# Kernel tuning notes

Hardware: AMD Instinct MI355X
Metric: run time of the kernel (lower is better)

Reference implementation:

```python
import jax, jax.numpy as jnp
import numpy as np
from jax import lax

B, T, D_LAT, D, H, J = 2048, 60, 100, 512, 256, 6
LRELU_SLOPE = 0.2
BN_EPS = 1e-5

# --- fixed kinematic-chain constants (stand-in for URDF: 6-DoF right arm) ---
AXES = np.array([[0,0,1],[1,0,0],[0,1,0],[1,0,0],[0,1,0],[1,0,0]], np.float32)
OFFS = np.array([[0,0,0.10],[0,0,0],[0,0,0],[0,-0.25,0],[0,0,0],[0,-0.25,0]], np.float32)
LOWER = np.array([-3.1416,-1.5708,-3.1416,-2.6,-1.5708,-1.2], np.float32)
UPPER = np.array([ 3.1416, 1.5708, 3.1416, 0.1, 1.5708, 1.2], np.float32)
FING1 = np.array([0.0,-0.08, 0.02], np.float32)
FING4 = np.array([0.0,-0.08,-0.02], np.float32)

def _skew(a):
    return np.array([[0,-a[2],a[1]],[a[2],0,-a[0]],[-a[1],a[0],0]], np.float32)

def fk_batch(joints):
    """joints: [B,T,6] normalized in [0,1]-ish -> poses [B,T,3,3]."""
    th = joints * (UPPER - LOWER) + LOWER                      # denormalize
    bt = th.shape[:2]
    R = jnp.broadcast_to(jnp.eye(3, dtype=th.dtype), bt + (3, 3))
    p = jnp.zeros(bt + (3,), th.dtype)
    pos = []
    for j in range(J):
        K = jnp.asarray(_skew(AXES[j]))
        a = th[..., j][..., None, None]
        Rj = jnp.eye(3, dtype=th.dtype) + jnp.sin(a) * K + (1.0 - jnp.cos(a)) * (K @ K)
        p = p + jnp.einsum('btij,j->bti', R, jnp.asarray(OFFS[j]))  # Trans then Rot
        R = jnp.einsum('btij,btjk->btik', R, Rj)
        pos.append(p)
    shoulder2, forearm, wrist = pos[1], pos[3], pos[5]
    f1 = wrist + jnp.einsum('btij,j->bti', R, jnp.asarray(FING1))
    f4 = wrist + jnp.einsum('btij,j->bti', R, jnp.asarray(FING4))
    body_L = (jnp.linalg.norm(shoulder2 - forearm, axis=-1)
              + jnp.linalg.norm(wrist - forearm, axis=-1)) * 0.5   # [B,T]
    rel = jnp.stack([wrist - shoulder2, f1 - shoulder2, f4 - shoulder2], axis=2)
    return rel / body_L[..., None, None]

def gru_dir(x, Wih, Whh, bih, bhh, reverse):
    xg = jnp.einsum('btd,gd->btg', x, Wih) + bih               # [B,T,3H]
    xg = jnp.swapaxes(xg, 0, 1)                                 # [T,B,3H]
    def step(h, g):
        gh = h @ Whh.T + bhh
        r = jax.nn.sigmoid(g[:, :H] + gh[:, :H])
        zz = jax.nn.sigmoid(g[:, H:2*H] + gh[:, H:2*H])
        n = jnp.tanh(g[:, 2*H:] + r * gh[:, 2*H:])
        hn = (1.0 - zz) * n + zz * h
        return hn, hn
    h0 = jnp.zeros((x.shape[0], H), x.dtype)
    _, ys = lax.scan(step, h0, xg, reverse=reverse)
    return jnp.swapaxes(ys, 0, 1)                               # [B,T,H]

def setup_inputs() -> dict:
    key = jax.random.key(0)
    ks = jax.random.split(key, 12)
    s = 0.05
    inp = {
        'z': jax.random.normal(ks[0], (B, D_LAT), jnp.float32),
        'W_fc': jax.random.normal(ks[1], (D, D_LAT), jnp.float32) * s,
        'b_fc': jnp.zeros((D,), jnp.float32),
        'bn_g': jnp.ones((D,), jnp.float32),
        'bn_b': jnp.zeros((D,), jnp.float32),
        'Wih_f': jax.random.normal(ks[2], (3*H, D), jnp.float32) * s,
        'Whh_f': jax.random.normal(ks[3], (3*H, H), jnp.float32) * s,
        'bih_f': jnp.zeros((3*H,), jnp.float32),
        'bhh_f': jnp.zeros((3*H,), jnp.float32),
        'Wih_b': jax.random.normal(ks[4], (3*H, D), jnp.float32) * s,
        'Whh_b': jax.random.normal(ks[5], (3*H, H), jnp.float32) * s,
        'bih_b': jnp.zeros((3*H,), jnp.float32),
        'bhh_b': jnp.zeros((3*H,), jnp.float32),
        'attn_W1': jax.random.normal(ks[6], (H, 2*H), jnp.float32) * s,
        'attn_b1': jnp.zeros((H,), jnp.float32),
        'attn_W2': jax.random.normal(ks[7], (H,), jnp.float32) * s,
        'joint_W': jax.random.normal(ks[8], (J, 2*H), jnp.float32) * s,
        'joint_b': jnp.zeros((J,), jnp.float32),
    }
    return inp

def reference(z, W_fc, b_fc, bn_g, bn_b, Wih_f, Whh_f, bih_f, bhh_f,
              Wih_b, Whh_b, bih_b, bhh_b, attn_W1, attn_b1, attn_W2,
              joint_W, joint_b):
    # fc: Linear + BatchNorm1d (training-mode batch stats) + LeakyReLU(0.2)
    h0 = z @ W_fc.T + b_fc                                      # [B,512]
    mu = jnp.mean(h0, axis=0)
    var = jnp.mean((h0 - mu) ** 2, axis=0)
    hb = (h0 - mu) * jax.lax.rsqrt(var + BN_EPS) * bn_g + bn_b
    h = jnp.where(hb >= 0, hb, LRELU_SLOPE * hb)
    x = jnp.broadcast_to(h[:, None, :], (h.shape[0], T, D))     # repeat over seq
    # bidirectional GRU
    gf = gru_dir(x, Wih_f, Whh_f, bih_f, bhh_f, False)
    gb = gru_dir(x, Wih_b, Whh_b, bih_b, bhh_b, True)
    gru_out = jnp.concatenate([gf, gb], axis=-1)                # [B,T,512]
    # attention over time
    a = jnp.tanh(jnp.einsum('btd,hd->bth', gru_out, attn_W1) + attn_b1)
    w = jax.nn.softmax(jnp.einsum('bth,h->bt', a, attn_W2), axis=1)[..., None]
    c = jnp.sum(w * gru_out, axis=1, keepdims=True)             # [B,1,512]
    joints = jnp.einsum('btd,jd->btj', gru_out + c, joint_W) + joint_b
    return fk_batch(joints)                                     # [B,T,3,3]
```

## Files before the change

### kernel.cpp

```cpp
#include <hip/hip_runtime.h>
#include <hip/hip_fp16.h>

#define NB 2048
#define NT 60
#define NDL 100
#define ND 512
#define NH 256
#define NG 768

#define L2E  1.44269504f
#define L2E2 2.88539008f

typedef const float* __restrict__ fpp;
typedef _Float16 half8 __attribute__((ext_vector_type(8)));
typedef float floatx4 __attribute__((ext_vector_type(4)));

__device__ __forceinline__ float fast_rcp(float x) {
  return __builtin_amdgcn_rcpf(x);
}
__device__ __forceinline__ float fast_exp2(float x) {
#if __has_builtin(__builtin_amdgcn_exp2f)
  return __builtin_amdgcn_exp2f(x);
#else
  return exp2f(x);
#endif
}
__device__ __forceinline__ float fsin(float x) {
#if __has_builtin(__builtin_amdgcn_sinf)
  return __builtin_amdgcn_sinf(x * 0.15915494309189535f);
#else
  return __sinf(x);
#endif
}
__device__ __forceinline__ float fcos(float x) {
#if __has_builtin(__builtin_amdgcn_cosf)
  return __builtin_amdgcn_cosf(x * 0.15915494309189535f);
#else
  return __cosf(x);
#endif
}

__global__ __launch_bounds__(256) void gemm_fc(
    fpp A, fpp Bm, fpp bias, float* __restrict__ C,
    int M, int N, int K, int lda, int ldb, int ldc)
{
  __shared__ float As[16][68];
  __shared__ float Bs[16][68];
  const int bm = blockIdx.x * 64, bn = blockIdx.y * 64;
  const int tid = threadIdx.x;
  const int tx = tid & 15, ty = tid >> 4;
  float acc[4][4] = {};
  for (int k0 = 0; k0 < K; k0 += 16) {
#pragma unroll
    for (int i = 0; i < 4; i++) {
      int e = tid + i * 256;
      int m = e >> 4, k = e & 15;
      As[k][m] = (k0 + k < K) ? A[(size_t)(bm + m) * lda + k0 + k] : 0.f;
      Bs[k][m] = (k0 + k < K) ? Bm[(size_t)(bn + m) * ldb + k0 + k] : 0.f;
    }
    __syncthreads();
#pragma unroll
    for (int kk = 0; kk < 16; kk++) {
      float4 av = *(const float4*)&As[kk][ty * 4];
      float4 bv = *(const float4*)&Bs[kk][tx * 4];
      float a_[4] = {av.x, av.y, av.z, av.w};
      float b_[4] = {bv.x, bv.y, bv.z, bv.w};
#pragma unroll
      for (int i = 0; i < 4; i++)
#pragma unroll
        for (int j = 0; j < 4; j++)
          acc[i][j] = fmaf(a_[i], b_[j], acc[i][j]);
    }
    __syncthreads();
  }
#pragma unroll
  for (int i = 0; i < 4; i++) {
    int m = bm + ty * 4 + i;
#pragma unroll
    for (int j = 0; j < 4; j++) {
      int n = bn + tx * 4 + j;
      C[(size_t)m * ldc + n] = acc[i][j] + bias[n];
    }
  }
}

__global__ __launch_bounds__(256) void bn_partial(
    const float* __restrict__ h0, float* __restrict__ s1g,
    float* __restrict__ s2g)
{
  const int r0 = blockIdx.x * 32;
  const int tid = threadIdx.x;
  float a1 = 0.f, a2 = 0.f, b1 = 0.f, b2 = 0.f;
  for (int r = 0; r < 32; r++) {
    float v = h0[(size_t)(r0 + r) * ND + tid];
    float w = h0[(size_t)(r0 + r) * ND + tid + 256];
    a1 += v; a2 += v * v;
    b1 += w; b2 += w * w;
  }
  atomicAdd(&s1g[tid], a1);
  atomicAdd(&s2g[tid], a2);
  atomicAdd(&s1g[tid + 256], b1);
  atomicAdd(&s2g[tid + 256], b2);
}

__global__ void bn_lrelu_h16(const float* __restrict__ h0,
                             fpp g, fpp b,
                             const float* __restrict__ s1g,
                             const float* __restrict__ s2g,
                             __half* __restrict__ h16g)
{
  int idx = blockIdx.x * 256 + threadIdx.x;
  int d = idx & (ND - 1);
  float mu = s1g[d] * (1.f / NB);
  float var = s2g[d] * (1.f / NB) - mu * mu;
  float sc = g[d] * rsqrtf(var + 1e-5f);
  float sh = b[d] - mu * sc;
  float v = h0[idx] * sc + sh;
  h16g[idx] = __float2half(v >= 0.f ? v : 0.2f * v);
}

__global__ void convert_w(fpp whf, fpp whb, fpp w1, fpp wif, fpp wib, fpp jw,
                          __half* __restrict__ o_whf, __half* __restrict__ o_whb,
                          __half* __restrict__ o_w1, __half* __restrict__ o_wif,
                          __half* __restrict__ o_wib, __half* __restrict__ o_jw)
{
  int idx = blockIdx.x * 256 + threadIdx.x;
  if (idx < 196608) {
    float s = ((idx >> 16) == 2) ? L2E2 : L2E;
    o_whf[idx] = __float2half(whf[idx] * s);
  } else if (idx < 393216) {
    int e = idx - 196608;
    float s = ((e >> 16) == 2) ? L2E2 : L2E;
    o_whb[e] = __float2half(whb[e] * s);
  } else if (idx < 524288) {
    int e = idx - 393216;
    o_w1[e] = __float2half(w1[e] * L2E2);
  } else if (idx < 917504) {
    int e = idx - 524288;
    float s = ((e >> 17) == 2) ? L2E2 : L2E;
    o_wif[e] = __float2half(wif[e] * s);
  } else if (idx < 1310720) {
    int e = idx - 917504;
    float s = ((e >> 17) == 2) ? L2E2 : L2E;
    o_wib[e] = __float2half(wib[e] * s);
  } else if (idx < 1318912) {
    int e = idx - 1310720;
    o_jw[e] = (e < 6 * ND) ? __float2half(jw[e]) : __float2half(0.f);
  }
}

__global__ __launch_bounds__(256) void gemm16_dual(
    const __half* __restrict__ A,
    const __half* __restrict__ B0, const __half* __restrict__ B1,
    fpp bias0, fpp bias1, float* __restrict__ C0, float* __restrict__ C1,
    int N, int K)
{
  const __half* __restrict__ Bm = blockIdx.z ? B1 : B0;
  fpp bias = blockIdx.z ? bias1 : bias0;
  float* __restrict__ C = blockIdx.z ? C1 : C0;

  __shared__ __half As[64 * 40];
  __shared__ __half Bs[64 * 40];
  const int bm = blockIdx.x * 64, bn = blockIdx.y * 64;
  const int tid = threadIdx.x;
  const int wave = tid >> 6, lane = tid & 63;
  const int lm = lane & 15, quad = lane >> 4;
  floatx4 acc[4];
#pragma unroll
  for (int nt = 0; nt < 4; nt++) acc[nt] = (floatx4){0.f, 0.f, 0.f, 0.f};

  const int row = tid >> 2, kc = tid & 3;
  for (int k0 = 0; k0 < K; k0 += 32) {
    __syncthreads();
    *(float4*)&As[row * 40 + kc * 8] =
      *(const float4*)&A[(size_t)(bm + row) * K + k0 + kc * 8];
    *(float4*)&Bs[row * 40 + kc * 8] =
      *(const float4*)&Bm[(size_t)(bn + row) * K + k0 + kc * 8];
    __syncthreads();
    half8 af = *(const half8*)&As[(wave * 16 + lm) * 40 + quad * 8];
#pragma unroll
    for (int nt = 0; nt < 4; nt++) {
      half8 bf = *(const half8*)&Bs[(nt * 16 + lm) * 40 + quad * 8];
      acc[nt] = __builtin_amdgcn_mfma_f32_16x16x32_f16(af, bf, acc[nt], 0, 0, 0);
    }
  }
#pragma unroll
  for (int nt = 0; nt < 4; nt++) {
    int n = bn + nt * 16 + lm;
    float bv = bias[n] * ((n < 2 * NH) ? L2E : L2E2);
#pragma unroll
    for (int r = 0; r < 4; r++) {
      int m = bm + wave * 16 + quad * 4 + r;
      C[(size_t)m * N + n] = acc[nt][r] + bv;
    }
  }
}

__global__ __launch_bounds__(512, 2) void gru_persistent(
    const float* __restrict__ xg_f, const float* __restrict__ xg_b,
    const __half* __restrict__ whh16_f, const __half* __restrict__ whh16_b,
    fpp bhh_f, fpp bhh_b, __half* __restrict__ seq)
{
  const int dir  = blockIdx.x & 1;
  const int tile = blockIdx.x >> 1;
  const int bm   = tile * 16;
  const float* __restrict__ xg = dir ? xg_b : xg_f;
  const __half* __restrict__ Whh = dir ? whh16_b : whh16_f;
  fpp bhh = dir ? bhh_b : bhh_f;
  const int dcol = dir * NH;
  const int tid = threadIdx.x;
  const int wave = tid >> 6, lane = tid & 63;
  const int lm = lane & 15, quad = lane >> 4;
  const int n0 = wave * 32;

  __shared__ __half h16s[2][16 * 264];
  __shared__ __half wts[96 * 512];

  floatx4 breg[3][2][6];
  {
    const __half* bp[3][2];
#pragma unroll
    for (int g = 0; g < 3; g++)
#pragma unroll
      for (int c = 0; c < 2; c++)
        bp[g][c] = Whh + (size_t)(g * NH + n0 + c * 16 + lm) * NH + quad * 8;

#pragma unroll
    for (int g = 0; g < 3; g++)
#pragma unroll
      for (int c = 0; c < 2; c++)
#pragma unroll
        for (int kb = 0; kb < 6; kb++)
          breg[g][c][kb] = *(const floatx4*)(bp[g][c] + kb * 32);
#pragma unroll
    for (int g = 0; g < 3; g++)
#pragma unroll
      for (int c = 0; c < 2; c++)
#pragma unroll
        for (int kb = 0; kb < 6; kb++)
          asm volatile("" : "+v"(breg[g][c][kb]));

#pragma unroll
    for (int g = 0; g < 3; g++)
#pragma unroll
      for (int c = 0; c < 2; c++)
#pragma unroll
        for (int k2 = 0; k2 < 2; k2++)
          *(float4*)&wts[(wave * 12 + g * 4 + c * 2 + k2) * 512 + lane * 8] =
            *(const float4*)(bp[g][c] + 192 + k2 * 32);
  }

  float xr_[2][4], xz_[2][4], xn_[2][4];
  float bn_[2];
#pragma unroll
  for (int c = 0; c < 2; c++) {
    int n = n0 + c * 16 + lm;
    float br = bhh[n] * L2E, bz = bhh[NH + n] * L2E;
    bn_[c] = bhh[2 * NH + n] * L2E2;
#pragma unroll
    for (int r = 0; r < 4; r++) {
      int m = bm + quad * 4 + r;
      const float* xp = xg + (size_t)m * NG + n;
      xr_[c][r] = xp[0] + br;
      xz_[c][r] = xp[NH] + bz;
      xn_[c][r] = xp[2 * NH];
    }
  }

  float hp[2][4];
#pragma unroll
  for (int c = 0; c < 2; c++)
#pragma unroll
    for (int r = 0; r < 4; r++) hp[c][r] = 0.f;

  const int arow = lm * 264 + quad * 8;
  const int cm = tid >> 5, cpart = tid & 31;
  const int wb = wave * 6144 + lane * 8;

  __half* seqp = seq + ((size_t)(bm + cm) * NT + (dir ? NT - 1 : 0)) * ND
                 + dcol + cpart * 8;
  const ptrdiff_t seqd = dir ? -(ptrdiff_t)ND : (ptrdiff_t)ND;

  for (int step = 0; step < NT; step++) {
    const int cur = step & 1, prv = cur ^ 1;
    __half* __restrict__ hCur = h16s[cur];
    const __half* __restrict__ hPrv = h16s[prv];
    floatx4 acc[3][2];

    if (step > 0) {
      {
        float4 v = *(const float4*)&hPrv[cm * 264 + cpart * 8];
        *(float4*)seqp = v;
        seqp += seqd;
      }
      half8 b6[3][2], b7[3][2];
#pragma unroll
      for (int g = 0; g < 3; g++)
#pragma unroll
        for (int c = 0; c < 2; c++) {
          const __half* wp = &wts[wb + (g * 4 + c * 2) * 512];
          b6[g][c] = *(const half8*)wp;
          b7[g][c] = *(const half8*)(wp + 512);
        }
      {
        half8 a = *(const half8*)&hPrv[arow];
#pragma unroll
        for (int g = 0; g < 3; g++)
#pragma unroll
          for (int c = 0; c < 2; c++)
            acc[g][c] = __builtin_amdgcn_mfma_f32_16x16x32_f16(
                a, __builtin_bit_cast(half8, breg[g][c][0]),
                (floatx4){0.f, 0.f, 0.f, 0.f}, 0, 0, 0);
      }
#pragma unroll
      for (int kb = 1; kb < 6; kb++) {
        half8 a = *(const half8*)&hPrv[arow + kb * 32];
#pragma unroll
        for (int g = 0; g < 3; g++)
#pragma unroll
          for (int c = 0; c < 2; c++)
            acc[g][c] = __builtin_amdgcn_mfma_f32_16x16x32_f16(
                a, __builtin_bit_cast(half8, breg[g][c][kb]), acc[g][c], 0, 0, 0);
      }
      {
        half8 a = *(const half8*)&hPrv[arow + 192];
#pragma unroll
        for (int g = 0; g < 3; g++)
#pragma unroll
          for (int c = 0; c < 2; c++)
            acc[g][c] = __builtin_amdgcn_mfma_f32_16x16x32_f16(a, b6[g][c], acc[g][c], 0, 0, 0);
      }
      {
        half8 a = *(const half8*)&hPrv[arow + 224];
#pragma unroll
        for (int g = 0; g < 3; g++)
#pragma unroll
          for (int c = 0; c < 2; c++)
            acc[g][c] = __builtin_amdgcn_mfma_f32_16x16x32_f16(a, b7[g][c], acc[g][c], 0, 0, 0);
      }
    } else {
#pragma unroll
      for (int g = 0; g < 3; g++)
#pragma unroll
        for (int c = 0; c < 2; c++) acc[g][c] = (floatx4){0.f, 0.f, 0.f, 0.f};
    }

#pragma unroll
    for (int c = 0; c < 2; c++) {
      int n = n0 + c * 16 + lm;
#pragma unroll
      for (int r = 0; r < 4; r++) {
        int m = quad * 4 + r;
        float rg = fast_rcp(1.f + fast_exp2(-(xr_[c][r] + acc[0][c][r])));
        float zg = fast_rcp(1.f + fast_exp2(-(xz_[c][r] + acc[1][c][r])));
        float t  = fast_exp2(fmaf(rg, acc[2][c][r] + bn_[c], xn_[c][r]));
        float nn = fmaf(-2.f, fast_rcp(t + 1.f), 1.f);
        float hv = fmaf(zg, hp[c][r] - nn, nn);
        hp[c][r] = hv;
        hCur[m * 264 + n] = __float2half(hv);
      }
    }
    __syncthreads();
  }

  {
    const __half* hLast = h16s[(NT - 1) & 1];
    float4 v = *(const float4*)&hLast[cm * 264 + cpart * 8];
    *(float4*)seqp = v;
  }
}

__global__ __launch_bounds__(256) void attn_score_mfma(
    const __half* __restrict__ seq, const __half* __restrict__ w116,
    const __half* __restrict__ jw16, fpp b1, fpp W2,
    float* __restrict__ scores, float* __restrict__ gJ)
{
  const int bm = blockIdx.x * 128;
  const int tid = threadIdx.x;
  const int wave = tid >> 6, lane = tid & 63;
  const int lm = lane & 15, quad = lane >> 4;
  const int mh = wave & 1;
  const int nh = wave >> 1;

  __shared__ __half As[128 * 40];
  __shared__ __half Bs[256 * 40];
  __shared__ __half Js[16 * 40];
  __shared__ float partial[2][128];

  floatx4 acc[4][8];
  floatx4 accJ[4];
#pragma unroll
  for (int t = 0; t < 4; t++) {
#pragma unroll
    for (int u = 0; u < 8; u++) acc[t][u] = (floatx4){0.f, 0.f, 0.f, 0.f};
    accJ[t] = (floatx4){0.f, 0.f, 0.f, 0.f};
  }

  for (int k0 = 0; k0 < ND; k0 += 32) {
    __syncthreads();
#pragma unroll
    for (int i = 0; i < 2; i++) {
      int e = tid + i * 256;
      int row = e >> 2, kc = e & 3;
      *(float4*)&As[row * 40 + kc * 8] =
        *(const float4*)&seq[(size_t)(bm + row) * ND + k0 + kc * 8];
    }
#pragma unroll
    for (int i = 0; i < 4; i++) {
      int e = tid + i * 256;
      int row = e >> 2, kc = e & 3;
      *(float4*)&Bs[row * 40 + kc * 8] =
        *(const float4*)&w116[(size_t)row * ND + k0 + kc * 8];
    }
    if (tid < 64) {
      int row = tid >> 2, kc = tid & 3;
      *(float4*)&Js[row * 40 + kc * 8] =
        *(const float4*)&jw16[(size_t)row * ND + k0 + kc * 8];
    }
    __syncthreads();
    half8 a[4];
#pragma unroll
    for (int t = 0; t < 4; t++)
      a[t] = *(const half8*)&As[((mh * 4 + t) * 16 + lm) * 40 + quad * 8];
#pragma unroll
    for (int u = 0; u < 8; u++) {
      half8 bf = *(const half8*)&Bs[((nh * 8 + u) * 16 + lm) * 40 + quad * 8];
#pragma unroll
      for (int t = 0; t < 4; t++)
        acc[t][u] = __builtin_amdgcn_mfma_f32_16x16x32_f16(a[t], bf, acc[t][u], 0, 0, 0);
    }
    if (nh == 1) {
      half8 bj = *(const half8*)&Js[lm * 40 + quad * 8];
#pragma unroll
      for (int t = 0; t < 4; t++)
        accJ[t] = __builtin_amdgcn_mfma_f32_16x16x32_f16(a[t], bj, accJ[t], 0, 0, 0);
    }
  }

  float rs[4][4] = {};
#pragma unroll
  for (int u = 0; u < 8; u++) {
    int n = (nh * 8 + u) * 16 + lm;
    float b1v = b1[n] * L2E2, w2v = W2[n];
#pragma unroll
    for (int t = 0; t < 4; t++)
#pragma unroll
      for (int r = 0; r < 4; r++) {
        float tt = fast_exp2(acc[t][u][r] + b1v);
        float th = fmaf(-2.f, fast_rcp(tt + 1.f), 1.f);
        rs[t][r] = fmaf(th, w2v, rs[t][r]);
      }
  }
#pragma unroll
  for (int t = 0; t < 4; t++)
#pragma unroll
    for (int r = 0; r < 4; r++) {
      rs[t][r] += __shfl_xor(rs[t][r], 1);
      rs[t][r] += __shfl_xor(rs[t][r], 2);
      rs[t][r] += __shfl_xor(rs[t][r], 4);
      rs[t][r] += __shfl_xor(rs[t][r], 8);
    }
  if (lm == 0) {
#pragma unroll
    for (int t = 0; t < 4; t++)
#pragma unroll
      for (int r = 0; r < 4; r++)
        partial[nh][mh * 64 + t * 16 + quad * 4 + r] = rs[t][r];
  }
  if (nh == 1) {
#pragma unroll
    for (int t = 0; t < 4; t++)
#pragma unroll
      for (int r = 0; r < 4; r++) {
        int row = bm + mh * 64 + t * 16 + quad * 4 + r;
        gJ[(size_t)row * 16 + lm] = accJ[t][r];
      }
  }
  __syncthreads();
  if (tid < 128) scores[bm + tid] = partial[0][tid] + partial[1][tid];
}

__constant__ float c_lower[6] = {-3.1416f, -1.5708f, -3.1416f, -2.6f, -1.5708f, -1.2f};
__constant__ float c_upper[6] = { 3.1416f,  1.5708f,  3.1416f,  0.1f,  1.5708f,  1.2f};

__global__ __launch_bounds__(64) void attn_post(
    const float* __restrict__ scores_in, const float* __restrict__ gJ,
    fpp jb, float* __restrict__ out)
{
  const int b = blockIdx.x;
  const int t = threadIdx.x;

  float v = (t < NT) ? scores_in[(size_t)b * NT + t] : -1e30f;
  float m = v;
#pragma unroll
  for (int off = 32; off >= 1; off >>= 1) m = fmaxf(m, __shfl_xor(m, off));
  float e = (t < NT) ? __expf(v - m) : 0.f;
  float sum = e;
#pragma unroll
  for (int off = 32; off >= 1; off >>= 1) sum += __shfl_xor(sum, off);
  float w = e * fast_rcp(sum);

  __shared__ float gj[NT * 16];
  __shared__ float wl[64];
  __shared__ float cj[16];
  wl[t] = w;
  const float* gsrc = gJ + (size_t)b * NT * 16;
#pragma unroll
  for (int i = 0; i < 15; i++) gj[t + i * 64] = gsrc[t + i * 64];
  __syncthreads();

  if (t < 16) {
    float s = 0.f;
    for (int tt = 0; tt < NT; tt++) s += wl[tt] * gj[tt * 16 + t];
    cj[t] = s;
  }
  __syncthreads();

  if (t >= NT) return;

  float th[6];
#pragma unroll
  for (int j = 0; j < 6; j++) {
    float jnt = gj[t * 16 + j] + cj[j] + jb[j];
    th[j] = jnt * (c_upper[j] - c_lower[j]) + c_lower[j];
  }

  float c0x = 1.f, c0y = 0.f, c0z = 0.f;
  float c1x = 0.f, c1y = 1.f, c1z = 0.f;
  float c2x = 0.f, c2y = 0.f, c2z = 1.f;
  float px = 0.f, py = 0.f, pz = 0.1f;
  float s, cc, tx_, ty_, tz_, ux_, uy_, uz_;

  s = fsin(th[0]); cc = fcos(th[0]);
  tx_ = cc * c0x + s * c1x; ty_ = cc * c0y + s * c1y; tz_ = cc * c0z + s * c1z;
  ux_ = -s * c0x + cc * c1x; uy_ = -s * c0y + cc * c1y; uz_ = -s * c0z + cc * c1z;
  c0x = tx_; c0y = ty_; c0z = tz_; c1x = ux_; c1y = uy_; c1z = uz_;

  float shx = px, shy = py, shz = pz;
  s = fsin(th[1]); cc = fcos(th[1]);
  tx_ = cc * c1x + s * c2x; ty_ = cc * c1y + s * c2y; tz_ = cc * c1z + s * c2z;
  ux_ = -s * c1x + cc * c2x; uy_ = -s * c1y + cc * c2y; uz_ = -s * c1z + cc * c2z;
  c1x = tx_; c1y = ty_; c1z = tz_; c2x = ux_; c2y = uy_; c2z = uz_;

  s = fsin(th[2]); cc = fcos(th[2]);
  tx_ = cc * c0x - s * c2x; ty_ = cc * c0y - s * c2y; tz_ = cc * c0z - s * c2z;
  ux_ = s * c0x + cc * c2x; uy_ = s * c0y + cc * c2y; uz_ = s * c0z + cc * c2z;
  c0x = tx_; c0y = ty_; c0z = tz_; c2x = ux_; c2y = uy_; c2z = uz_;

  px -= 0.25f * c1x; py -= 0.25f * c1y; pz -= 0.25f * c1z;
  float fox = px, foy = py, foz = pz;
  s = fsin(th[3]); cc = fcos(th[3]);
  tx_ = cc * c1x + s * c2x; ty_ = cc * c1y + s * c2y; tz_ = cc * c1z + s * c2z;
  ux_ = -s * c1x + cc * c2x; uy_ = -s * c1y + cc * c2y; uz_ = -s * c1z + cc * c2z;
  c1x = tx_; c1y = ty_; c1z = tz_; c2x = ux_; c2y = uy_; c2z = uz_;

  s = fsin(th[4]); cc = fcos(th[4]);
  tx_ = cc * c0x - s * c2x; ty_ = cc * c0y - s * c2y; tz_ = cc * c0z - s * c2z;
  ux_ = s * c0x + cc * c2x; uy_ = s * c0y + cc * c2y; uz_ = s * c0z + cc * c2z;
  c0x = tx_; c0y = ty_; c0z = tz_; c2x = ux_; c2y = uy_; c2z = uz_;

  px -= 0.25f * c1x; py -= 0.25f * c1y; pz -= 0.25f * c1z;
  float wx = px, wy = py, wz = pz;
  s = fsin(th[5]); cc = fcos(th[5]);
  tx_ = cc * c1x + s * c2x; ty_ = cc * c1y + s * c2y; tz_ = cc * c1z + s * c2z;
  ux_ = -s * c1x + cc * c2x; uy_ = -s * c1y + cc * c2y; uz_ = -s * c1z + cc * c2z;
  c1x = tx_; c1y = ty_; c1z = tz_; c2x = ux_; c2y = uy_; c2z = uz_;

  float f1x = wx - 0.08f * c1x + 0.02f * c2x;
  float f1y = wy - 0.08f * c1y + 0.02f * c2y;
  float f1z = wz - 0.08f * c1z + 0.02f * c2z;
  float f4x = wx - 0.08f * c1x - 0.02f * c2x;
  float f4y = wy - 0.08f * c1y - 0.02f * c2y;
  float f4z = wz - 0.08f * c1z - 0.02f * c2z;

  float dsx = shx - fox, dsy = shy - foy, dsz = shz - foz;
  float dwx = wx - fox, dwy = wy - foy, dwz = wz - foz;
  float bodyL = 0.5f * (sqrtf(dsx * dsx + dsy * dsy + dsz * dsz) +
                        sqrtf(dwx * dwx + dwy * dwy + dwz * dwz));
  float inv = fast_rcp(bodyL);

  float* o = out + ((size_t)b * NT + t) * 9;
  o[0] = (wx - shx) * inv; o[1] = (wy - shy) * inv; o[2] = (wz - shz) * inv;
  o[3] = (f1x - shx) * inv; o[4] = (f1y - shy) * inv; o[5] = (f1z - shz) * inv;
  o[6] = (f4x - shx) * inv; o[7] = (f4y - shy) * inv; o[8] = (f4z - shz) * inv;
}

extern "C" void kernel_launch(void* const* d_in, const int* in_sizes, int n_in,
                              void* d_out, int out_size, void* d_ws, size_t ws_size,
                              hipStream_t stream)
{
  fpp z     = (fpp)d_in[0];
  fpp W_fc  = (fpp)d_in[1];
  fpp b_fc  = (fpp)d_in[2];
  fpp bn_g  = (fpp)d_in[3];
  fpp bn_b  = (fpp)d_in[4];
  fpp Wih_f = (fpp)d_in[5];
  fpp Whh_f = (fpp)d_in[6];
  fpp bih_f = (fpp)d_in[7];
  fpp bhh_f = (fpp)d_in[8];
  fpp Wih_b = (fpp)d_in[9];
  fpp Whh_b = (fpp)d_in[10];
  fpp bih_b = (fpp)d_in[11];
  fpp bhh_b = (fpp)d_in[12];
  fpp aW1   = (fpp)d_in[13];
  fpp ab1   = (fpp)d_in[14];
  fpp aW2   = (fpp)d_in[15];
  fpp jW    = (fpp)d_in[16];
  fpp jb    = (fpp)d_in[17];

  float* ws     = (float*)d_ws;
  float* h0     = ws;
  float* xg_f   = h0 + 1048576;
  float* xg_b   = xg_f + 1572864;
  float* bns1   = xg_b + 1572864;
  float* bns2   = bns1 + 512;
  float* scores = bns2 + 512;
  float* cbuf   = scores + 122880;
  __half* gseq    = (__half*)(cbuf + 1048576);
  __half* whh16_f = gseq + 62914560;
  __half* whh16_b = whh16_f + 196608;
  __half* w116    = whh16_b + 196608;
  __half* wih16_f = w116 + 131072;
  __half* wih16_b = wih16_f + 393216;
  __half* h16g    = wih16_b + 393216;
  __half* jw16    = h16g + 1048576;
  float*  gJ      = (float*)(jw16 + 8192);

  convert_w<<<5152, 256, 0, stream>>>(Whh_f, Whh_b, aW1, Wih_f, Wih_b, jW,
                                      whh16_f, whh16_b, w116, wih16_f, wih16_b,
                                      jw16);
  hipMemsetAsync(bns1, 0, 1024 * sizeof(float), stream);
  gemm_fc<<<dim3(32, 8), 256, 0, stream>>>(z, W_fc, b_fc, h0,
                                           NB, ND, NDL, NDL, NDL, ND);
  bn_partial<<<64, 256, 0, stream>>>(h0, bns1, bns2);
  bn_lrelu_h16<<<4096, 256, 0, stream>>>(h0, bn_g, bn_b, bns1, bns2, h16g);
  gemm16_dual<<<dim3(32, 12, 2), 256, 0, stream>>>(
      h16g, wih16_f, wih16_b, bih_f, bih_b, xg_f, xg_b, NG, ND);
  gru_persistent<<<256, 512, 0, stream>>>(xg_f, xg_b, whh16_f, whh16_b,
                                          bhh_f, bhh_b, gseq);
  attn_score_mfma<<<960, 256, 0, stream>>>(gseq, w116, jw16, ab1, aW2,
                                           scores, gJ);
  attn_post<<<NB, 64, 0, stream>>>(scores, gJ, jb, (float*)d_out);
}
```

Baseline: 330.6 us.

## Interleave GRU matmul chains with gate math and prefetch attention tiles

The GRU recurrence now preloads the x-gate terms and hidden bias into the MFMA accumulators and runs the matmul for column chunk 0, then its gates, then chunk 1 and its gates. s_setprio is used so one wave's gate math can overlap another wave's MFMAs. The gate formula is rewritten algebraically to use fewer reciprocals. The attention-score kernel register-prefetches the next K tile from global memory while the current tile is being computed. The aim is to shorten the serial per-step critical path and hide global load latency, at the cost of more registers and changed fp rounding.

```diff
diff --git a/kernel.cpp b/kernel.cpp
--- a/kernel.cpp
+++ b/kernel.cpp
@@ -196,6 +196,47 @@
   }
 }
 
+#define GATES(C) do {                                                        \
+    _Pragma("unroll")                                                        \
+    for (int r = 0; r < 4; r++) {                                            \
+      float er = fast_exp2(-acc[0][C][r]);                                   \
+      float rg = fast_rcp(1.f + er);                                         \
+      float ez = fast_exp2(-acc[1][C][r]);                                   \
+      float tt = fast_exp2(fmaf(rg, acc[2][C][r], xn4[C][r]));               \
+      float dd = tt + 1.f;                                                   \
+      float num = fmaf(tt, ez + hp[C][r], hp[C][r] - ez);                    \
+      float den = fmaf(dd, ez, dd);                                          \
+      float hv = num * fast_rcp(den);                                        \
+      hp[C][r] = hv;                                                         \
+      hCur[(quad * 4 + r) * 264 + (n0 + C * 16 + lm)] = __float2half(hv);    \
+    }                                                                        \
+  } while (0)
+
+#define CHAIN(C) do {                                                        \
+    half8 t6[3], t7[3];                                                      \
+    _Pragma("unroll")                                                        \
+    for (int g = 0; g < 3; g++) {                                            \
+      const __half* wp = &wts[wb + (g * 4 + C * 2) * 512];                   \
+      t6[g] = *(const half8*)wp;                                             \
+      t7[g] = *(const half8*)(wp + 512);                                     \
+    }                                                                        \
+    _Pragma("unroll")                                                        \
+    for (int kb = 0; kb < 6; kb++)                                           \
+      _Pragma("unroll")                                                      \
+      for (int g = 0; g < 3; g++)                                            \
+        acc[g][C] = __builtin_amdgcn_mfma_f32_16x16x32_f16(                  \
+            a[kb], __builtin_bit_cast(half8, breg[g][C][kb]), acc[g][C],     \
+            0, 0, 0);                                                        \
+    _Pragma("unroll")                                                        \
+    for (int g = 0; g < 3; g++)                                              \
+      acc[g][C] = __builtin_amdgcn_mfma_f32_16x16x32_f16(                    \
+          a[6], t6[g], acc[g][C], 0, 0, 0);                                  \
+    _Pragma("unroll")                                                        \
+    for (int g = 0; g < 3; g++)                                              \
+      acc[g][C] = __builtin_amdgcn_mfma_f32_16x16x32_f16(                    \
+          a[7], t7[g], acc[g][C], 0, 0, 0);                                  \
+  } while (0)
+
 __global__ __launch_bounds__(512, 2) void gru_persistent(
     const float* __restrict__ xg_f, const float* __restrict__ xg_b,
     const __half* __restrict__ whh16_f, const __half* __restrict__ whh16_b,
@@ -250,7 +291,7 @@
             *(const float4*)(bp[g][c] + 192 + k2 * 32);
   }
 
-  float xr_[2][4], xz_[2][4], xn_[2][4];
+  floatx4 xr4[2], xz4[2], xn4[2];
   float bn_[2];
 #pragma unroll
   for (int c = 0; c < 2; c++) {
@@ -261,9 +302,9 @@
     for (int r = 0; r < 4; r++) {
       int m = bm + quad * 4 + r;
       const float* xp = xg + (size_t)m * NG + n;
-      xr_[c][r] = xp[0] + br;
-      xz_[c][r] = xp[NH] + bz;
-      xn_[c][r] = xp[2 * NH];
+      xr4[c][r] = xp[0] + br;
+      xz4[c][r] = xp[NH] + bz;
+      xn4[c][r] = xp[2 * NH];
     }
   }
 
@@ -286,6 +327,12 @@
     __half* __restrict__ hCur = h16s[cur];
     const __half* __restrict__ hPrv = h16s[prv];
     floatx4 acc[3][2];
+#pragma unroll
+    for (int c = 0; c < 2; c++) {
+      acc[0][c] = xr4[c];
+      acc[1][c] = xz4[c];
+      acc[2][c] = (floatx4){bn_[c], bn_[c], bn_[c], bn_[c]};
+    }
 
     if (step > 0) {
       {
@@ -293,72 +340,22 @@
         *(float4*)seqp = v;
         seqp += seqd;
       }
-      half8 b6[3][2], b7[3][2];
-#pragma unroll
-      for (int g = 0; g < 3; g++)
-#pragma unroll
-        for (int c = 0; c < 2; c++) {
-          const __half* wp = &wts[wb + (g * 4 + c * 2) * 512];
-          b6[g][c] = *(const half8*)wp;
-          b7[g][c] = *(const half8*)(wp + 512);
-        }
-      {
-        half8 a = *(const half8*)&hPrv[arow];
-#pragma unroll
-        for (int g = 0; g < 3; g++)
-#pragma unroll
-          for (int c = 0; c < 2; c++)
-            acc[g][c] = __builtin_amdgcn_mfma_f32_16x16x32_f16(
-                a, __builtin_bit_cast(half8, breg[g][c][0]),
-                (floatx4){0.f, 0.f, 0.f, 0.f}, 0, 0, 0);
-      }
-#pragma unroll
-      for (int kb = 1; kb < 6; kb++) {
-        half8 a = *(const half8*)&hPrv[arow + kb * 32];
-#pragma unroll
-        for (int g = 0; g < 3; g++)
-#pragma unroll
-          for (int c = 0; c < 2; c++)
-            acc[g][c] = __builtin_amdgcn_mfma_f32_16x16x32_f16(
-                a, __builtin_bit_cast(half8, breg[g][c][kb]), acc[g][c], 0, 0, 0);
-      }
-      {
-        half8 a = *(const half8*)&hPrv[arow + 192];
-#pragma unroll
-        for (int g = 0; g < 3; g++)
-#pragma unroll
-          for (int c = 0; c < 2; c++)
-            acc[g][c] = __builtin_amdgcn_mfma_f32_16x16x32_f16(a, b6[g][c], acc[g][c], 0, 0, 0);
-      }
-      {
-        half8 a = *(const half8*)&hPrv[arow + 224];
-#pragma unroll
-        for (int g = 0; g < 3; g++)
-#pragma unroll
-          for (int c = 0; c < 2; c++)
-            acc[g][c] = __builtin_amdgcn_mfma_f32_16x16x32_f16(a, b7[g][c], acc[g][c], 0, 0, 0);
-      }
+      half8 a[8];
+#pragma unroll
+      for (int kb = 0; kb < 8; kb++)
+        a[kb] = *(const half8*)&hPrv[arow + kb * 32];
+
+      __builtin_amdgcn_s_setprio(1);
+      CHAIN(0);
+      __builtin_amdgcn_s_setprio(0);
+      GATES(0);
+      __builtin_amdgcn_s_setprio(1);
+      CHAIN(1);
+      __builtin_amdgcn_s_setprio(0);
+      GATES(1);
     } else {
-#pragma unroll
-      for (int g = 0; g < 3; g++)
-#pragma unroll
-        for (int c = 0; c < 2; c++) acc[g][c] = (floatx4){0.f, 0.f, 0.f, 0.f};
-    }
-
-#pragma unroll
-    for (int c = 0; c < 2; c++) {
-      int n = n0 + c * 16 + lm;
-#pragma unroll
-      for (int r = 0; r < 4; r++) {
-        int m = quad * 4 + r;
-        float rg = fast_rcp(1.f + fast_exp2(-(xr_[c][r] + acc[0][c][r])));
-        float zg = fast_rcp(1.f + fast_exp2(-(xz_[c][r] + acc[1][c][r])));
-        float t  = fast_exp2(fmaf(rg, acc[2][c][r] + bn_[c], xn_[c][r]));
-        float nn = fmaf(-2.f, fast_rcp(t + 1.f), 1.f);
-        float hv = fmaf(zg, hp[c][r] - nn, nn);
-        hp[c][r] = hv;
-        hCur[m * 264 + n] = __float2half(hv);
-      }
+      GATES(0);
+      GATES(1);
     }
     __syncthreads();
   }
@@ -396,28 +393,32 @@
     accJ[t] = (floatx4){0.f, 0.f, 0.f, 0.f};
   }
 
+  const int srow = tid >> 2, skc8 = (tid & 3) * 8;
+  float4 pa[2], pb[4], pj = {};
+
+#define LOADK(K0) do {                                                       \
+    _Pragma("unroll")                                                        \
+    for (int i = 0; i < 2; i++)                                              \
+      pa[i] = *(const float4*)&seq[(size_t)(bm + srow + i * 64) * ND + (K0) + skc8]; \
+    _Pragma("unroll")                                                        \
+    for (int i = 0; i < 4; i++)                                              \
+      pb[i] = *(const float4*)&w116[(size_t)(srow + i * 64) * ND + (K0) + skc8];     \
+    if (tid < 64) pj = *(const float4*)&jw16[(size_t)srow * ND + (K0) + skc8];       \
+  } while (0)
+
+  LOADK(0);
   for (int k0 = 0; k0 < ND; k0 += 32) {
     __syncthreads();
 #pragma unroll
-    for (int i = 0; i < 2; i++) {
-      int e = tid + i * 256;
-      int row = e >> 2, kc = e & 3;
-      *(float4*)&As[row * 40 + kc * 8] =
-        *(const float4*)&seq[(size_t)(bm + row) * ND + k0 + kc * 8];
-    }
-#pragma unroll
-    for (int i = 0; i < 4; i++) {
-      int e = tid + i * 256;
-      int row = e >> 2, kc = e & 3;
-      *(float4*)&Bs[row * 40 + kc * 8] =
-        *(const float4*)&w116[(size_t)row * ND + k0 + kc * 8];
-    }
-    if (tid < 64) {
-      int row = tid >> 2, kc = tid & 3;
-      *(float4*)&Js[row * 40 + kc * 8] =
-        *(const float4*)&jw16[(size_t)row * ND + k0 + kc * 8];
-    }
+    for (int i = 0; i < 2; i++)
+      *(float4*)&As[(srow + i * 64) * 40 + skc8] = pa[i];
+#pragma unroll
+    for (int i = 0; i < 4; i++)
+      *(float4*)&Bs[(srow + i * 64) * 40 + skc8] = pb[i];
+    if (tid < 64) *(float4*)&Js[srow * 40 + skc8] = pj;
+    if (k0 + 32 < ND) LOADK(k0 + 32);
     __syncthreads();
+
     half8 a[4];
 #pragma unroll
     for (int t = 0; t < 4; t++)
@@ -436,6 +437,7 @@
         accJ[t] = __builtin_amdgcn_mfma_f32_16x16x32_f16(a[t], bj, accJ[t], 0, 0, 0);
     }
   }
+#undef LOADK
 
   float rs[4][4] = {};
 #pragma unroll
```

Result: slower. 373.5 us (+13.0%).
